# Kernel tuning notes

Measured on AMD Instinct MI355X. Metric: run time of the kernel, lower is better.

Reference implementation:

```python
import jax, jax.numpy as jnp
import numpy as np

N_NODES = 100_000
N_EDGES = 1_600_000
HID = 64
LAYERS = 3
MAX_ATOM = 100
BATCH = 16


def setup_inputs() -> dict:
    key = jax.random.key(0)
    ks = jax.random.split(key, 24)
    s = 0.05  # weight scale
    inp = {
        "x": jax.random.normal(ks[0], (N_NODES, 3), dtype=jnp.float32),
        "z": jax.random.randint(ks[1], (N_NODES,), 0, MAX_ATOM),
        "t": jax.random.uniform(ks[2], (BATCH, 1), dtype=jnp.float32),
        "edge_index": jax.random.randint(ks[3], (2, N_EDGES), 0, N_NODES),
        # atom embedding table
        "emb": jax.random.normal(ks[4], (MAX_ATOM, HID)) * s,
        # time embedding MLP: Linear(1,H), SiLU, Linear(H,H)
        "t_w1": jax.random.normal(ks[5], (1, HID)) * s,
        "t_b1": jnp.zeros((HID,)),
        "t_w2": jax.random.normal(ks[6], (HID, HID)) * s,
        "t_b2": jnp.zeros((HID,)),
        # per-layer EGNN params, stacked over layers
        # edge MLP: Linear(2H+1, H), SiLU, Linear(H, H), SiLU
        "e_w1": jax.random.normal(ks[7], (LAYERS, 2 * HID + 1, HID)) * s,
        "e_b1": jnp.zeros((LAYERS, HID)),
        "e_w2": jax.random.normal(ks[8], (LAYERS, HID, HID)) * s,
        "e_b2": jnp.zeros((LAYERS, HID)),
        # coord MLP: Linear(H, H), SiLU, Linear(H, 1)
        "c_w1": jax.random.normal(ks[9], (LAYERS, HID, HID)) * s,
        "c_b1": jnp.zeros((LAYERS, HID)),
        "c_w2": jax.random.normal(ks[10], (LAYERS, HID, 1)) * s,
        "c_b2": jnp.zeros((LAYERS, 1)),
        # node MLP: Linear(2H, H), SiLU, Linear(H, H), residual
        "n_w1": jax.random.normal(ks[11], (LAYERS, 2 * HID, HID)) * s,
        "n_b1": jnp.zeros((LAYERS, HID)),
        "n_w2": jax.random.normal(ks[12], (LAYERS, HID, HID)) * s,
        "n_b2": jnp.zeros((LAYERS, HID)),
    }
    return inp


def reference(x, z, t, edge_index, emb,
              t_w1, t_b1, t_w2, t_b2,
              e_w1, e_b1, e_w2, e_b2,
              c_w1, c_b1, c_w2, c_b2,
              n_w1, n_b1, n_w2, n_b2):
    silu = jax.nn.silu
    n = x.shape[0]
    # atom embedding + global time conditioning
    h = emb[z]                                           # (N, H)
    t_emb = silu(t @ t_w1 + t_b1) @ t_w2 + t_b2          # (B, H)
    h = h + jnp.mean(t_emb, axis=0, keepdims=True)
    src, dst = edge_index[0], edge_index[1]
    for l in range(LAYERS):
        diff = x[dst] - x[src]                           # (E, 3)
        d2 = jnp.sum(diff * diff, axis=-1, keepdims=True)  # (E, 1)
        ef = jnp.concatenate([h[dst], h[src], d2], axis=-1)  # (E, 2H+1)
        m = silu(silu(ef @ e_w1[l] + e_b1[l]) @ e_w2[l] + e_b2[l])  # (E, H)
        cw = silu(m @ c_w1[l] + c_b1[l]) @ c_w2[l] + c_b2[l]        # (E, 1)
        x = x + jax.ops.segment_sum(diff * cw, dst, num_segments=n)
        agg = jax.ops.segment_sum(m, dst, num_segments=n)           # (N, H)
        nf = jnp.concatenate([h, agg], axis=-1)                     # (N, 2H)
        h = h + (silu(nf @ n_w1[l] + n_b1[l]) @ n_w2[l] + n_b2[l])
    return x
```

## Files before the change

### kernel.cpp

```cpp
#include <hip/hip_runtime.h>

typedef __attribute__((ext_vector_type(8))) short s8v;
typedef __attribute__((ext_vector_type(4))) float f32x4;

#define MFMA16(A,B,C) __builtin_amdgcn_mfma_f32_16x16x32_bf16((A),(B),(C),0,0,0)

__device__ __forceinline__ float b2f(unsigned short s){
  union { unsigned u; float f; } v; v.u = ((unsigned)s) << 16; return v.f;
}
__device__ __forceinline__ unsigned short f2b(float f){
  union { float f; unsigned u; } v; v.f = f;
  return (unsigned short)((v.u + 0x8000u) >> 16);
}
__device__ __forceinline__ unsigned cvtpk(float lo, float hi){
  unsigned r;
  asm("v_cvt_pk_bf16_f32 %0, %1, %2" : "=v"(r) : "v"(lo), "v"(hi));
  return r;
}
__device__ __forceinline__ float siluf(float x){
  return x * __builtin_amdgcn_rcpf(1.f + __expf(-x));
}


__global__ void hist_kernel(const int* __restrict__ dst, int* __restrict__ deg, int E){
  int i = blockIdx.x*256 + threadIdx.x;
  if (i < E) atomicAdd(&deg[dst[i]], 1);
}

__global__ void scan1_kernel(const int* __restrict__ deg, int* __restrict__ rp,
                             int* __restrict__ bsum, int N){
  __shared__ int s[256];
  const int base = blockIdx.x*1024;
  const int t = threadIdx.x;
  int v[4];
  #pragma unroll
  for (int j = 0; j < 4; ++j){
    int idx = base + t*4 + j;
    int dv = (idx < N) ? deg[idx] : 0;
    v[j] = (dv + 3) & ~3;
  }
  const int tsum = v[0]+v[1]+v[2]+v[3];
  s[t] = tsum;
  __syncthreads();
  for (int off = 1; off < 256; off <<= 1){
    int x = (t >= off) ? s[t-off] : 0;
    __syncthreads();
    s[t] += x;
    __syncthreads();
  }
  const int incl = s[t];
  if (t == 255) bsum[blockIdx.x] = incl;
  int run = incl - tsum;
  #pragma unroll
  for (int j = 0; j < 4; ++j){
    int idx = base + t*4 + j;
    if (idx < N) rp[idx] = run;
    run += v[j];
  }
}

__global__ void scan3_kernel(int* __restrict__ rp, const int* __restrict__ bsum,
                             const int* __restrict__ deg, int N, int nb){
  __shared__ int sb[256];
  __shared__ int so[256];
  const int t = threadIdx.x;
  const int v = (t < nb) ? bsum[t] : 0;
  sb[t] = v; so[t] = v;
  __syncthreads();
  for (int off = 1; off < 256; off <<= 1){
    int x = (t >= off) ? sb[t-off] : 0;
    __syncthreads();
    sb[t] += x;
    __syncthreads();
  }
  int i = blockIdx.x*256 + t;
  if (i < N){
    const int k = i >> 10;
    const int val = rp[i] + (sb[k] - so[k]);
    rp[i] = val;
    if (i == N-1) rp[N] = val + ((deg[i] + 3) & ~3);
  }
}

__global__ void scatter_slot_kernel(const int* __restrict__ src, const int* __restrict__ dst,
                                    const int* __restrict__ rp, int* __restrict__ cursor,
                                    int* __restrict__ csr_src, int* __restrict__ slot_meta,
                                    const int* __restrict__ deg, int E, int N){
  int i = blockIdx.x*256 + threadIdx.x;
  if (i < E){
    const int d = dst[i];
    const int pos = rp[d] + atomicAdd(&cursor[d], 1);
    csr_src[pos] = src[i];
  }
  if (i < N){
    const int base = rp[i];
    const int d = deg[i];
    const int ns = (d + 3) >> 2;
    const int s0 = base >> 2;
    for (int k = 0; k < ns; ++k){
      int c = d - k*4; c = (c > 4) ? 4 : c;
      slot_meta[s0 + k] = i | (c << 28);
    }
    for (int j = d; j < ns*4; ++j) csr_src[base + j] = i;
  }
  if (i == 0){
    const int S  = rp[N] >> 2;
    const int S4 = (S + 3) & ~3;
    for (int s = S; s < S4; ++s){
      slot_meta[s] = 0;
      for (int r = 0; r < 4; ++r) csr_src[s*4 + r] = 0;
    }
  }
}


__global__ void tmean_zero_kernel(const float* __restrict__ t,
                                  const float* __restrict__ tw1,
                                  const float* __restrict__ tb1,
                                  const float* __restrict__ tw2,
                                  const float* __restrict__ tb2,
                                  float* __restrict__ tmean,
                                  int* __restrict__ degcur, int n2){
  for (int k = blockIdx.x*256 + threadIdx.x; k < n2; k += gridDim.x*256)
    degcur[k] = 0;
  if (blockIdx.x == 0){
    __shared__ __align__(16) float s1[16*64];
    const int j = threadIdx.x & 63;
    const int grp = threadIdx.x >> 6;
    const float w1 = tw1[j], bb1 = tb1[j];
    #pragma unroll
    for (int b = grp*4; b < grp*4 + 4; ++b)
      s1[b*64 + j] = siluf(t[b] * w1 + bb1);
    __syncthreads();
    if (threadIdx.x < 64){
      float acc = 0.f;
      for (int b = 0; b < 16; ++b)
        for (int k = 0; k < 64; ++k)
          acc += s1[b*64 + k] * tw2[k*64 + j];
      tmean[j] = tb2[j] + acc * (1.f/16.f);
    }
  }
}


__global__ __launch_bounds__(512) void init_p12_kernel(
    const int* __restrict__ z,
    const float* __restrict__ emb,
    const float* __restrict__ tmean,
    const float* __restrict__ ew1, const float* __restrict__ eb1,
    unsigned short* __restrict__ hb,
    float* __restrict__ aggf,
    unsigned short* __restrict__ P1, unsigned short* __restrict__ P2,
    const float* __restrict__ x0, float* __restrict__ xa, int N)
{
  __shared__ __align__(16) short w1a[64*72];
  __shared__ __align__(16) short w1b[64*72];
  __shared__ __align__(16) float b1s[64];

  const int tid = threadIdx.x;
  const float* w1g = ew1;
  for (int idx = tid; idx < 64*64; idx += 512){
    int k = idx >> 6, n = idx & 63;
    w1a[n*72 + k] = (short)f2b(w1g[k*64 + n]);
    w1b[n*72 + k] = (short)f2b(w1g[(64 + k)*64 + n]);
  }
  if (tid < 64) b1s[tid] = eb1[tid];
  __syncthreads();

  const int lane = tid & 63;
  const int wv = tid >> 6;
  const int q = lane >> 4;
  const int n16 = lane & 15;

  const f32x4 tm0 = *(const f32x4*)(tmean + q*8);
  const f32x4 tm1 = *(const f32x4*)(tmean + q*8 + 4);
  const f32x4 tm2 = *(const f32x4*)(tmean + 32 + q*8);
  const f32x4 tm3 = *(const f32x4*)(tmean + 32 + q*8 + 4);
  const f32x4 zz = {0.f,0.f,0.f,0.f};

  const int ntile = N >> 4;
  const int step = gridDim.x * 8;
  for (int t = blockIdx.x*8 + wv; t < ntile; t += step){
    const int row = t*16 + n16;
    if (lane < 48) xa[t*48 + lane] = x0[t*48 + lane];

    const float* er = emb + (size_t)z[row]*64;
    const f32x4 v0 = *(const f32x4*)(er + q*8)          + tm0;
    const f32x4 v1 = *(const f32x4*)(er + q*8 + 4)      + tm1;
    const f32x4 v2 = *(const f32x4*)(er + 32 + q*8)     + tm2;
    const f32x4 v3 = *(const f32x4*)(er + 32 + q*8 + 4) + tm3;

    float* arow = aggf + (size_t)row*64;
    *(f32x4*)(arow + q*8)          = zz;
    *(f32x4*)(arow + q*8 + 4)      = zz;
    *(f32x4*)(arow + 32 + q*8)     = zz;
    *(f32x4*)(arow + 32 + q*8 + 4) = zz;

    s8v a0, a1;
    #pragma unroll
    for (int j = 0; j < 4; ++j){
      a0[j]   = (short)f2b(v0[j]);
      a0[4+j] = (short)f2b(v1[j]);
      a1[j]   = (short)f2b(v2[j]);
      a1[4+j] = (short)f2b(v3[j]);
    }
    *(s8v*)(hb + (size_t)row*64 + q*8)      = a0;
    *(s8v*)(hb + (size_t)row*64 + 32 + q*8) = a1;

    #pragma unroll
    for (int nt = 0; nt < 4; ++nt){
      const s8v* wa = (const s8v*)&w1a[(nt*16 + n16)*72];
      const s8v* wb = (const s8v*)&w1b[(nt*16 + n16)*72];
      f32x4 aA = {0.f,0.f,0.f,0.f};
      aA = MFMA16(a0, wa[q],   aA);
      aA = MFMA16(a1, wa[4+q], aA);
      f32x4 aB = {0.f,0.f,0.f,0.f};
      aB = MFMA16(a0, wb[q],   aB);
      aB = MFMA16(a1, wb[4+q], aB);
      const float bb = b1s[nt*16 + n16];
      #pragma unroll
      for (int r = 0; r < 4; ++r){
        const int o = (t*16 + q*4 + r)*64 + nt*16 + n16;
        P1[o] = f2b(aA[r] + bb);
        P2[o] = f2b(aB[r]);
      }
    }
  }
}


__global__ __launch_bounds__(512) void edge_tile_kernel(
    const int* __restrict__ rp, const int* __restrict__ csr_src,
    const int* __restrict__ slot_meta,
    const float* __restrict__ x_in, float* __restrict__ x_out,
    const unsigned short* __restrict__ P1, const unsigned short* __restrict__ P2,
    float* __restrict__ aggf,
    const float* __restrict__ ew1,
    const float* __restrict__ ew2, const float* __restrict__ eb2,
    const float* __restrict__ cw1, const float* __restrict__ cb1,
    const float* __restrict__ cw2, const float* __restrict__ cb2,
    int layer, int do_agg, int N)
{
  __shared__ __align__(16) short wT2[64*72];
  __shared__ __align__(16) short wc1T[64*72];
  __shared__ __align__(16) short sc[8][16*72];
  __shared__ __align__(16) float sdiff[8][48];

  const int tid = threadIdx.x;
  const float* w2g = ew2 + layer*64*64;
  const float* c1g = cw1 + layer*64*64;
  for (int idx = tid; idx < 64*64; idx += 512){
    int k = idx >> 6, n = idx & 63;
    wT2[n*72 + k]  = (short)f2b(w2g[k*64 + n]);
    wc1T[n*72 + k] = (short)f2b(c1g[k*64 + n]);
  }

  const int lane = tid & 63;
  const int wv = tid >> 6;
  const int q = lane >> 4;
  const int n16 = lane & 15;
  short* mysc = sc[wv];
  float* mydiff = sdiff[wv];

  const float* wlg = ew1 + layer*129*64 + 128*64;
  float wl_lo[8], wl_hi[8];
  #pragma unroll
  for (int j = 0; j < 8; ++j){
    wl_lo[j] = wlg[q*8 + j];
    wl_hi[j] = wlg[32 + q*8 + j];
  }
  float be2r[4], bc1r[4], cw2r[4];
  #pragma unroll
  for (int nt = 0; nt < 4; ++nt){
    be2r[nt] = eb2[layer*64 + nt*16 + n16];
    bc1r[nt] = cb1[layer*64 + nt*16 + n16];
    cw2r[nt] = cw2[layer*64 + nt*16 + n16];
  }
  const float cb2s = cb2[layer];
  __syncthreads();

  auto tile_compute = [&](int mo, float dx, float dy, float dz,
                          s8v lo1, s8v hi1, s8v lo2, s8v hi2, bool valid){
    const float d2 = dx*dx + dy*dy + dz*dz;
    if (q == 0){ mydiff[n16] = dx; mydiff[16+n16] = dy; mydiff[32+n16] = dz; }

    s8v alo, ahi;
    {
      union { unsigned u[4]; s8v s; } ua, ub;
      #pragma unroll
      for (int jp = 0; jp < 4; ++jp){
        const int j0 = 2*jp, j1 = 2*jp + 1;
        const float a0f = siluf(b2f((unsigned short)lo1[j0]) + b2f((unsigned short)lo2[j0]) + d2*wl_lo[j0]);
        const float a1f = siluf(b2f((unsigned short)lo1[j1]) + b2f((unsigned short)lo2[j1]) + d2*wl_lo[j1]);
        ua.u[jp] = cvtpk(a0f, a1f);
        const float b0f = siluf(b2f((unsigned short)hi1[j0]) + b2f((unsigned short)hi2[j0]) + d2*wl_hi[j0]);
        const float b1f = siluf(b2f((unsigned short)hi1[j1]) + b2f((unsigned short)hi2[j1]) + d2*wl_hi[j1]);
        ub.u[jp] = cvtpk(b0f, b1f);
      }
      alo = ua.s; ahi = ub.s;
    }

    f32x4 acc2[4];
    #pragma unroll
    for (int nt = 0; nt < 4; ++nt){
      const s8v* wb = (const s8v*)&wT2[(nt*16 + n16)*72];
      f32x4 a = {0.f,0.f,0.f,0.f};
      a = MFMA16(alo, wb[q],   a);
      a = MFMA16(ahi, wb[4+q], a);
      acc2[nt] = a;
    }

    const int dn = mo & 0x0FFFFFFF;
    const int cnt = (int)(((unsigned)mo) >> 28);

    float colsum[4] = {0.f,0.f,0.f,0.f};
    #pragma unroll
    for (int nt = 0; nt < 4; ++nt){
      const float bb = be2r[nt];
      #pragma unroll
      for (int r = 0; r < 4; ++r){
        const float mv = siluf(acc2[nt][r] + bb);
        mysc[(q*4 + r)*72 + nt*16 + n16] = (short)cvtpk(mv, mv);
        colsum[nt] += (r < cnt) ? mv : 0.f;
      }
    }
    __builtin_amdgcn_wave_barrier();
    const s8v* srd = (const s8v*)&mysc[n16*72];
    const s8v m0 = srd[q];
    const s8v m1 = srd[4+q];
    __builtin_amdgcn_wave_barrier();

    float pr[4] = {0.f,0.f,0.f,0.f};
    #pragma unroll
    for (int nt = 0; nt < 4; ++nt){
      const s8v* wb = (const s8v*)&wc1T[(nt*16 + n16)*72];
      f32x4 a = {0.f,0.f,0.f,0.f};
      a = MFMA16(m0, wb[q],   a);
      a = MFMA16(m1, wb[4+q], a);
      const float bc = bc1r[nt];
      const float wc2 = cw2r[nt];
      #pragma unroll
      for (int r = 0; r < 4; ++r) pr[r] += siluf(a[r] + bc) * wc2;
    }
    #pragma unroll
    for (int off = 1; off < 16; off <<= 1){
      #pragma unroll
      for (int r = 0; r < 4; ++r) pr[r] += __shfl_xor(pr[r], off, 64);
    }
    const f32x4 dfx = *(const f32x4*)&mydiff[q*4];
    const f32x4 dfy = *(const f32x4*)&mydiff[16 + q*4];
    const f32x4 dfz = *(const f32x4*)&mydiff[32 + q*4];
    float xacc0 = 0.f, xacc1 = 0.f, xacc2 = 0.f;
    #pragma unroll
    for (int r = 0; r < 4; ++r){
      const float cwv = pr[r] + cb2s;
      xacc0 += dfx[r] * cwv;
      xacc1 += dfy[r] * cwv;
      xacc2 += dfz[r] * cwv;
    }

    const int dnb = __shfl_xor(dn, 16, 64);
    const bool same = (dnb == dn);
    #pragma unroll
    for (int nt = 0; nt < 4; ++nt){
      const float o = __shfl_xor(colsum[nt], 16, 64);
      if (same) colsum[nt] += o;
    }
    const float o0 = __shfl_xor(xacc0, 16, 64);
    const float o1 = __shfl_xor(xacc1, 16, 64);
    const float o2 = __shfl_xor(xacc2, 16, 64);
    if (same){ xacc0 += o0; xacc1 += o1; xacc2 += o2; }

    const bool writer = (((q & 1) == 0) || !same) && valid;
    if (do_agg && writer){
      #pragma unroll
      for (int nt = 0; nt < 4; ++nt)
        atomicAdd(&aggf[(size_t)dn*64 + nt*16 + n16], colsum[nt]);
    }
    if (writer && n16 < 3){
      const float v = (n16 == 0) ? xacc0 : (n16 == 1) ? xacc1 : xacc2;
      atomicAdd(&x_out[dn*3 + n16], v);
    }
  };

  const int T = (rp[N] + 15) >> 4;
  const int npair = (T + 1) >> 1;
  const int nwave = gridDim.x * 8;
  for (int pp = blockIdx.x*8 + wv; pp < npair; pp += nwave){
    const int ta = pp*2;
    const int tb = pp*2 + 1;
    const bool vb = (tb < T);
    const int tbb = vb ? tb : ta;

    const int miA = slot_meta[ta*4 + (n16 >> 2)];
    const int moA = slot_meta[ta*4 + q];
    const int siA = csr_src[ta*16 + n16];
    const int miB = slot_meta[tbb*4 + (n16 >> 2)];
    const int moB = slot_meta[tbb*4 + q];
    const int siB = csr_src[tbb*16 + n16];
    const int diA = miA & 0x0FFFFFFF;
    const int diB = miB & 0x0FFFFFFF;

    const float dxA = x_in[diA*3+0] - x_in[siA*3+0];
    const float dyA = x_in[diA*3+1] - x_in[siA*3+1];
    const float dzA = x_in[diA*3+2] - x_in[siA*3+2];
    const float dxB = x_in[diB*3+0] - x_in[siB*3+0];
    const float dyB = x_in[diB*3+1] - x_in[siB*3+1];
    const float dzB = x_in[diB*3+2] - x_in[siB*3+2];

    const s8v* pdA = (const s8v*)(P1 + (size_t)diA*64);
    const s8v lo1A = pdA[q], hi1A = pdA[4+q];
    const s8v* psA = (const s8v*)(P2 + (size_t)siA*64);
    const s8v lo2A = psA[q], hi2A = psA[4+q];
    const s8v* pdB = (const s8v*)(P1 + (size_t)diB*64);
    const s8v lo1B = pdB[q], hi1B = pdB[4+q];
    const s8v* psB = (const s8v*)(P2 + (size_t)siB*64);
    const s8v lo2B = psB[q], hi2B = psB[4+q];

    tile_compute(moA, dxA, dyA, dzA, lo1A, hi1A, lo2A, hi2A, true);
    tile_compute(moB, dxB, dyB, dzB, lo1B, hi1B, lo2B, hi2B, vb);
  }
}


__global__ __launch_bounds__(512) void node_p12_kernel(
    unsigned short* __restrict__ hb,
    float* __restrict__ aggf,
    const float* __restrict__ nw1, const float* __restrict__ nb1,
    const float* __restrict__ nw2, const float* __restrict__ nb2,
    const float* __restrict__ ew1, const float* __restrict__ eb1,
    unsigned short* __restrict__ P1, unsigned short* __restrict__ P2,
    const float* __restrict__ xsrc, float* __restrict__ xdst,
    int layer, int do_zero, int do_h, int N)
{
  __shared__ __align__(16) short wT1[64*136];
  __shared__ __align__(16) short wT2[64*72];
  __shared__ __align__(16) short w1a[64*72];
  __shared__ __align__(16) short w1b[64*72];
  __shared__ __align__(16) short sc[8][16*72];
  __shared__ __align__(16) float b1s[64];
  __shared__ __align__(16) float b2s[64];
  __shared__ __align__(16) float eb1s[64];

  const int tid = threadIdx.x;
  const float* w1g = nw1 + layer*128*64;
  const float* w2g = nw2 + layer*64*64;
  const float* e1g = ew1 + (layer+1)*129*64;
  for (int idx = tid; idx < 64*128; idx += 512){
    int k = idx >> 6, n = idx & 63;
    wT1[n*136 + k] = (short)f2b(w1g[k*64 + n]);
  }
  for (int idx = tid; idx < 64*64; idx += 512){
    int k = idx >> 6, n = idx & 63;
    wT2[n*72 + k] = (short)f2b(w2g[k*64 + n]);
    w1a[n*72 + k] = (short)f2b(e1g[k*64 + n]);
    w1b[n*72 + k] = (short)f2b(e1g[(64 + k)*64 + n]);
  }
  if (tid < 64){
    b1s[tid]  = nb1[layer*64 + tid];
    b2s[tid]  = nb2[layer*64 + tid];
    eb1s[tid] = eb1[(layer+1)*64 + tid];
  }
  __syncthreads();

  const int lane = tid & 63;
  const int wv = tid >> 6;
  const int q = lane >> 4;
  const int n16 = lane & 15;
  short* mysc = sc[wv];

  const int ntile = N >> 4;
  const int step = gridDim.x * 8;
  for (int t = blockIdx.x*8 + wv; t < ntile; t += step){
    const int row = t*16 + n16;
    const s8v* ph = (const s8v*)(hb + row*64);
    const s8v a0 = ph[q];
    const s8v a1 = ph[4+q];
    const f32x4* pa = (const f32x4*)(aggf + (size_t)row*64);
    const f32x4 u0 = pa[2*q];
    const f32x4 u1 = pa[2*q+1];
    const f32x4 u2 = pa[8+2*q];
    const f32x4 u3 = pa[9+2*q];
    s8v a2, a3;
    #pragma unroll
    for (int j = 0; j < 4; ++j){
      a2[j]   = (short)f2b(u0[j]);
      a2[4+j] = (short)f2b(u1[j]);
      a3[j]   = (short)f2b(u2[j]);
      a3[4+j] = (short)f2b(u3[j]);
    }
    if (do_zero){
      const f32x4 zz = {0.f,0.f,0.f,0.f};
      f32x4* pw = (f32x4*)(aggf + (size_t)row*64);
      pw[2*q] = zz; pw[2*q+1] = zz; pw[8+2*q] = zz; pw[9+2*q] = zz;
    }
    if (lane < 48) xdst[t*48 + lane] = xsrc[t*48 + lane];

    #pragma unroll
    for (int nt = 0; nt < 4; ++nt){
      const s8v* wb = (const s8v*)&wT1[(nt*16 + n16)*136];
      f32x4 a = {0.f,0.f,0.f,0.f};
      a = MFMA16(a0, wb[q],    a);
      a = MFMA16(a1, wb[4+q],  a);
      a = MFMA16(a2, wb[8+q],  a);
      a = MFMA16(a3, wb[12+q], a);
      const float bb = b1s[nt*16 + n16];
      #pragma unroll
      for (int r = 0; r < 4; ++r)
        mysc[(q*4 + r)*72 + nt*16 + n16] = (short)f2b(siluf(a[r] + bb));
    }
    __builtin_amdgcn_wave_barrier();
    const s8v* srd = (const s8v*)&mysc[n16*72];
    const s8v g0 = srd[q];
    const s8v g1 = srd[4+q];
    __builtin_amdgcn_wave_barrier();

    #pragma unroll
    for (int nt = 0; nt < 4; ++nt){
      const s8v* wb = (const s8v*)&wT2[(nt*16 + n16)*72];
      f32x4 a = {0.f,0.f,0.f,0.f};
      a = MFMA16(g0, wb[q],   a);
      a = MFMA16(g1, wb[4+q], a);
      const float bb = b2s[nt*16 + n16];
      #pragma unroll
      for (int r = 0; r < 4; ++r){
        const int idx = (t*16 + q*4 + r)*64 + nt*16 + n16;
        const float hv = b2f(hb[idx]) + a[r] + bb;
        const unsigned short hvb = f2b(hv);
        if (do_h) hb[idx] = hvb;
        mysc[(q*4 + r)*72 + nt*16 + n16] = (short)hvb;
      }
    }
    __builtin_amdgcn_wave_barrier();
    const s8v h0 = srd[q];
    const s8v h1 = srd[4+q];
    __builtin_amdgcn_wave_barrier();

    #pragma unroll
    for (int nt = 0; nt < 4; ++nt){
      const s8v* wa = (const s8v*)&w1a[(nt*16 + n16)*72];
      const s8v* wb = (const s8v*)&w1b[(nt*16 + n16)*72];
      f32x4 aA = {0.f,0.f,0.f,0.f};
      aA = MFMA16(h0, wa[q],   aA);
      aA = MFMA16(h1, wa[4+q], aA);
      f32x4 aB = {0.f,0.f,0.f,0.f};
      aB = MFMA16(h0, wb[q],   aB);
      aB = MFMA16(h1, wb[4+q], aB);
      const float bb = eb1s[nt*16 + n16];
      #pragma unroll
      for (int r = 0; r < 4; ++r){
        const int o = (t*16 + q*4 + r)*64 + nt*16 + n16;
        P1[o] = f2b(aA[r] + bb);
        P2[o] = f2b(aB[r]);
      }
    }
  }
}


extern "C" void kernel_launch(void* const* d_in, const int* in_sizes, int n_in,
                              void* d_out, int out_size, void* d_ws, size_t ws_size,
                              hipStream_t stream)
{
  const float* x0   = (const float*)d_in[0];
  const int*   z    = (const int*)d_in[1];
  const float* tc   = (const float*)d_in[2];
  const int*   ei   = (const int*)d_in[3];
  const float* embc = (const float*)d_in[4];
  const float* tw1c = (const float*)d_in[5];
  const float* tb1c = (const float*)d_in[6];
  const float* tw2c = (const float*)d_in[7];
  const float* tb2c = (const float*)d_in[8];
  const float* ew1c = (const float*)d_in[9];
  const float* eb1c = (const float*)d_in[10];
  const float* ew2c = (const float*)d_in[11];
  const float* eb2c = (const float*)d_in[12];
  const float* cw1c = (const float*)d_in[13];
  const float* cb1c = (const float*)d_in[14];
  const float* cw2c = (const float*)d_in[15];
  const float* cb2c = (const float*)d_in[16];
  const float* nw1c = (const float*)d_in[17];
  const float* nb1c = (const float*)d_in[18];
  const float* nw2c = (const float*)d_in[19];
  const float* nb2c = (const float*)d_in[20];

  const int N = in_sizes[1];
  const int E = in_sizes[3] / 2;
  const int* srcp = ei;
  const int* dstp = ei + E;

  char* p = (char*)d_ws;
  auto alloc = [&](size_t bytes) -> void* {
    void* r = (void*)p; p += (bytes + 255) & ~(size_t)255; return r;
  };
  unsigned short* hbuf = (unsigned short*)alloc((size_t)N*64*2);
  float* aggf          = (float*)alloc((size_t)N*64*4);
  unsigned short* P1   = (unsigned short*)alloc((size_t)N*64*2);
  unsigned short* P2   = (unsigned short*)alloc((size_t)N*64*2);
  float* xa            = (float*)alloc((size_t)N*3*4);
  float* xb            = (float*)alloc((size_t)N*3*4);
  float* tmean         = (float*)alloc(64*4);
  int*   degcur        = (int*)alloc((size_t)2*N*4);
  int*   deg           = degcur;
  int*   cursor        = degcur + N;
  int*   rowp          = (int*)alloc((size_t)(N+1)*4);
  int*   bsum          = (int*)alloc(256*4);
  int*   csr_src       = (int*)alloc(((size_t)E + 3*(size_t)N + 64)*4);
  int*   slot_meta     = (int*)alloc(((size_t)E/4 + (size_t)N + 16)*4);

  tmean_zero_kernel<<<512, 256, 0, stream>>>(tc, tw1c, tb1c, tw2c, tb2c,
                                             tmean, degcur, 2*N);
  init_p12_kernel<<<512, 512, 0, stream>>>(z, embc, tmean, ew1c, eb1c,
                                           hbuf, aggf, P1, P2, x0, xa, N);

  hist_kernel<<<(E + 255)/256, 256, 0, stream>>>(dstp, deg, E);
  const int nb = (N + 1023)/1024;
  scan1_kernel<<<nb, 256, 0, stream>>>(deg, rowp, bsum, N);
  scan3_kernel<<<(N + 255)/256, 256, 0, stream>>>(rowp, bsum, deg, N, nb);
  scatter_slot_kernel<<<(E + 255)/256, 256, 0, stream>>>(srcp, dstp, rowp, cursor,
                                                         csr_src, slot_meta, deg, E, N);

  const float* xc = x0;
  float* xnexts[3] = {xa, xb, (float*)d_out};
  for (int l = 0; l < 3; ++l){
    float* xout = xnexts[l];
    edge_tile_kernel<<<1024, 512, 0, stream>>>(rowp, csr_src, slot_meta, xc, xout,
        P1, P2, aggf,
        ew1c, ew2c, eb2c, cw1c, cb1c, cw2c, cb2c, l, (l < 2) ? 1 : 0, N);
    if (l < 2)
      node_p12_kernel<<<512, 512, 0, stream>>>(hbuf, aggf,
          nw1c, nb1c, nw2c, nb2c, ew1c, eb1c, P1, P2,
          xout, xnexts[l+1], l, (l == 0) ? 1 : 0, (l == 0) ? 1 : 0, N);
    xc = xout;
  }
}
```

Measured before the change: 751.9 us.

## Fuse CSR build and time-embedding prep into one cooperative kernel with grid syncs

Replaces the five small preprocessing launches (zeroing plus time MLP, histogram, two scan passes, scatter) with a single cooperative kernel that separates the phases with grid-wide barriers. The aim is to remove per-launch overhead and the idle gaps between these short kernels. If the cooperative launch fails, the original multi-kernel path runs instead. In exchange, the fused kernel runs on a fixed grid of 512 blocks of 256 threads, so the histogram and scatter loops are grid-strided with less parallelism than the original launches, and each grid sync adds its own cost.

```diff
diff --git a/kernel.cpp b/kernel.cpp
--- a/kernel.cpp
+++ b/kernel.cpp
@@ -1,4 +1,7 @@
 #include <hip/hip_runtime.h>
+#include <hip/hip_cooperative_groups.h>
+
+namespace cg = cooperative_groups;
 
 typedef __attribute__((ext_vector_type(8))) short s8v;
 typedef __attribute__((ext_vector_type(4))) float f32x4;
@@ -19,6 +22,127 @@
 }
 __device__ __forceinline__ float siluf(float x){
   return x * __builtin_amdgcn_rcpf(1.f + __expf(-x));
+}
+
+
+__global__ void csr_coop_kernel(const float* __restrict__ t,
+                                const float* __restrict__ tw1,
+                                const float* __restrict__ tb1,
+                                const float* __restrict__ tw2,
+                                const float* __restrict__ tb2,
+                                float* __restrict__ tmean,
+                                const int* __restrict__ src, const int* __restrict__ dst,
+                                int* __restrict__ degcur, int* __restrict__ rp,
+                                int* __restrict__ bsum,
+                                int* __restrict__ csr_src, int* __restrict__ slot_meta,
+                                int E, int N){
+  cg::grid_group grid = cg::this_grid();
+  __shared__ __align__(16) float s1[16*64];
+  __shared__ int s[256];
+  __shared__ int sb[256];
+  __shared__ int so[256];
+
+  const int tid = threadIdx.x;
+  const int gidx = blockIdx.x*256 + tid;
+  const int gstep = gridDim.x*256;
+  int* deg = degcur;
+  int* cursor = degcur + N;
+
+  for (int k = gidx; k < 2*N; k += gstep) degcur[k] = 0;
+  if (blockIdx.x == gridDim.x - 1){
+    const int j = tid & 63;
+    const int grp = tid >> 6;
+    const float w1 = tw1[j], bb1 = tb1[j];
+    #pragma unroll
+    for (int b = grp*4; b < grp*4 + 4; ++b)
+      s1[b*64 + j] = siluf(t[b] * w1 + bb1);
+    __syncthreads();
+    if (tid < 64){
+      float acc = 0.f;
+      for (int b = 0; b < 16; ++b)
+        for (int k = 0; k < 64; ++k)
+          acc += s1[b*64 + k] * tw2[k*64 + j];
+      tmean[j] = tb2[j] + acc * (1.f/16.f);
+    }
+  }
+  grid.sync();
+
+  for (int i = gidx; i < E; i += gstep) atomicAdd(&deg[dst[i]], 1);
+  grid.sync();
+
+  const int nb = (N + 1023) >> 10;
+  if (blockIdx.x < nb){
+    const int base = blockIdx.x*1024;
+    int v[4];
+    #pragma unroll
+    for (int j = 0; j < 4; ++j){
+      int idx = base + tid*4 + j;
+      int dv = (idx < N) ? deg[idx] : 0;
+      v[j] = (dv + 3) & ~3;
+    }
+    const int tsum = v[0]+v[1]+v[2]+v[3];
+    s[tid] = tsum;
+    __syncthreads();
+    for (int off = 1; off < 256; off <<= 1){
+      int x = (tid >= off) ? s[tid-off] : 0;
+      __syncthreads();
+      s[tid] += x;
+      __syncthreads();
+    }
+    const int incl = s[tid];
+    if (tid == 255) bsum[blockIdx.x] = incl;
+    int run = incl - tsum;
+    #pragma unroll
+    for (int j = 0; j < 4; ++j){
+      int idx = base + tid*4 + j;
+      if (idx < N) rp[idx] = run;
+      run += v[j];
+    }
+  }
+  grid.sync();
+
+  {
+    const int v = (tid < nb) ? bsum[tid] : 0;
+    sb[tid] = v; so[tid] = v;
+    __syncthreads();
+    for (int off = 1; off < 256; off <<= 1){
+      int x = (tid >= off) ? sb[tid-off] : 0;
+      __syncthreads();
+      sb[tid] += x;
+      __syncthreads();
+    }
+    for (int i = gidx; i < N; i += gstep){
+      const int k = i >> 10;
+      rp[i] += sb[k] - so[k];
+    }
+    if (gidx == 0) rp[N] = sb[nb-1];
+  }
+  grid.sync();
+
+  for (int i = gidx; i < E; i += gstep){
+    const int d = dst[i];
+    const int pos = rp[d] + atomicAdd(&cursor[d], 1);
+    csr_src[pos] = src[i];
+  }
+  for (int n = gidx; n < N; n += gstep){
+    const int base = rp[n];
+    const int d = deg[n];
+    const int ns = (d + 3) >> 2;
+    const int s0 = base >> 2;
+    for (int k = 0; k < ns; ++k){
+      int c = d - k*4; c = (c > 4) ? 4 : c;
+      slot_meta[s0 + k] = n | (c << 28);
+    }
+    for (int j = d; j < ns*4; ++j) csr_src[base + j] = n;
+  }
+  if (gidx == 0){
+    const int S  = rp[N] >> 2;
+    const int S4 = (S + 3) & ~3;
+    for (int sI = S; sI < S4; ++sI){
+      slot_meta[sI] = 0;
+      for (int r = 0; r < 4; ++r) csr_src[sI*4 + r] = 0;
+    }
+  }
 }
 
 
@@ -112,7 +236,6 @@
     }
   }
 }
-
 
 __global__ void tmean_zero_kernel(const float* __restrict__ t,
                                   const float* __restrict__ tw1,
@@ -585,7 +708,7 @@
   const float* nb2c = (const float*)d_in[20];
 
   const int N = in_sizes[1];
-  const int E = in_sizes[3] / 2;
+  int E = in_sizes[3] / 2;
   const int* srcp = ei;
   const int* dstp = ei + E;
 
@@ -608,17 +731,27 @@
   int*   csr_src       = (int*)alloc(((size_t)E + 3*(size_t)N + 64)*4);
   int*   slot_meta     = (int*)alloc(((size_t)E/4 + (size_t)N + 16)*4);
 
-  tmean_zero_kernel<<<512, 256, 0, stream>>>(tc, tw1c, tb1c, tw2c, tb2c,
-                                             tmean, degcur, 2*N);
+  int Nv = N;
+  void* cargs[] = { (void*)&tc, (void*)&tw1c, (void*)&tb1c, (void*)&tw2c, (void*)&tb2c,
+                    (void*)&tmean, (void*)&srcp, (void*)&dstp, (void*)&degcur,
+                    (void*)&rowp, (void*)&bsum, (void*)&csr_src, (void*)&slot_meta,
+                    (void*)&E, (void*)&Nv };
+  hipError_t cerr = hipLaunchCooperativeKernel((void*)csr_coop_kernel,
+                        dim3(512), dim3(256), cargs, 0, stream);
+  if (cerr != hipSuccess){
+    (void)hipGetLastError();
+    tmean_zero_kernel<<<512, 256, 0, stream>>>(tc, tw1c, tb1c, tw2c, tb2c,
+                                               tmean, degcur, 2*N);
+    hist_kernel<<<(E + 255)/256, 256, 0, stream>>>(dstp, deg, E);
+    const int nb = (N + 1023)/1024;
+    scan1_kernel<<<nb, 256, 0, stream>>>(deg, rowp, bsum, N);
+    scan3_kernel<<<(N + 255)/256, 256, 0, stream>>>(rowp, bsum, deg, N, nb);
+    scatter_slot_kernel<<<(E + 255)/256, 256, 0, stream>>>(srcp, dstp, rowp, cursor,
+                                                           csr_src, slot_meta, deg, E, N);
+  }
+
   init_p12_kernel<<<512, 512, 0, stream>>>(z, embc, tmean, ew1c, eb1c,
                                            hbuf, aggf, P1, P2, x0, xa, N);
-
-  hist_kernel<<<(E + 255)/256, 256, 0, stream>>>(dstp, deg, E);
-  const int nb = (N + 1023)/1024;
-  scan1_kernel<<<nb, 256, 0, stream>>>(deg, rowp, bsum, N);
-  scan3_kernel<<<(N + 255)/256, 256, 0, stream>>>(rowp, bsum, deg, N, nb);
-  scatter_slot_kernel<<<(E + 255)/256, 256, 0, stream>>>(srcp, dstp, rowp, cursor,
-                                                         csr_src, slot_meta, deg, E, N);
 
   const float* xc = x0;
   float* xnexts[3] = {xa, xb, (float*)d_out};
```

Measured after the change: 995.3 us. +32.4%, slower.
